# Kernel tuning notes

Measured on AMD Instinct MI355X. Metric: run time of the kernel, lower is better.

Reference implementation:

```python
import jax, jax.numpy as jnp
import numpy as np

D_MODEL = 1024
NUM_TILES = 64
TPC = 8                      # tiles_per_cluster
NUM_CLUSTERS = NUM_TILES // TPC
GRID = 16
COMP_H = 256                 # compress hidden = d_model // 4
NUM_KNOTS = 8
EPS_LN = 1e-5


def setup_inputs() -> dict:
    key = jax.random.key(0)
    ks = jax.random.split(key, 12)
    B, T = 4, 4096
    x = jax.random.normal(ks[0], (B, T, D_MODEL), dtype=jnp.float32)
    signatures_raw = jax.random.normal(ks[1], (NUM_TILES, D_MODEL), dtype=jnp.float32) * 0.5
    knot_values = jax.nn.sigmoid(jnp.linspace(-3.0, 3.0, NUM_KNOTS).astype(jnp.float32))
    temperature = jnp.ones((1,), dtype=jnp.float32)
    # compress: Linear(d,comp_h) -> GELU -> Linear(comp_h,2) -> Tanh
    compress_w1 = jax.random.normal(ks[2], (D_MODEL, COMP_H), dtype=jnp.float32) * (1.0 / np.sqrt(D_MODEL))
    compress_b1 = jnp.zeros((COMP_H,), dtype=jnp.float32)
    compress_w2 = jax.random.normal(ks[3], (COMP_H, 2), dtype=jnp.float32) * (1.0 / np.sqrt(COMP_H))
    compress_b2 = jnp.zeros((2,), dtype=jnp.float32)
    # per-tile magnitude splines: Linear(2,grid) -> ReLU -> Linear(grid,1)
    spline_w1 = jax.random.normal(ks[4], (NUM_TILES, 2, GRID), dtype=jnp.float32) * (1.0 / np.sqrt(2.0))
    spline_b1 = jnp.zeros((NUM_TILES, GRID), dtype=jnp.float32)
    spline_w2 = jax.random.normal(ks[5], (NUM_TILES, GRID, 1), dtype=jnp.float32) * (1.0 / np.sqrt(GRID))
    spline_b2 = jnp.zeros((NUM_TILES, 1), dtype=jnp.float32)
    directions = jax.random.normal(ks[6], (NUM_TILES, D_MODEL), dtype=jnp.float32) * 0.02
    norm_gamma = jnp.ones((D_MODEL,), dtype=jnp.float32)
    norm_beta = jnp.zeros((D_MODEL,), dtype=jnp.float32)
    output_scale = jnp.ones((1,), dtype=jnp.float32) * 0.1
    return dict(x=x, signatures_raw=signatures_raw, knot_values=knot_values,
                temperature=temperature, compress_w1=compress_w1, compress_b1=compress_b1,
                compress_w2=compress_w2, compress_b2=compress_b2, spline_w1=spline_w1,
                spline_b1=spline_b1, spline_w2=spline_w2, spline_b2=spline_b2,
                directions=directions, norm_gamma=norm_gamma, norm_beta=norm_beta,
                output_scale=output_scale)


def _calibrate(scores, knots, temperature):
    # ScoreCalibrationSpline: sigmoid -> linear interpolation over knots
    K = knots.shape[0]
    normalized = jax.nn.sigmoid(scores / (temperature[0] + 1e-6))
    idx_float = normalized * (K - 1)
    idx_low = jnp.clip(idx_float.astype(jnp.int32), 0, K - 2)
    idx_high = idx_low + 1
    t = idx_float - idx_low.astype(scores.dtype)
    val_low = knots[idx_low]
    val_high = knots[idx_high]
    return val_low + t * (val_high - val_low)


def _forward(x, signatures_raw, knot_values, temperature, compress_w1, compress_b1,
             compress_w2, compress_b2, spline_w1, spline_b1, spline_w2, spline_b2,
             directions, norm_gamma, norm_beta, output_scale):
    B, T, D = x.shape
    xf = x.reshape(-1, D)  # [N, D]

    # ternary quantized signatures with straight-through estimator
    q = jnp.where(signatures_raw > 0.3, 1.0,
                  jnp.where(signatures_raw < -0.3, -1.0, 0.0)).astype(signatures_raw.dtype)
    sigs = signatures_raw + jax.lax.stop_gradient(q - signatures_raw)  # [NT, D]

    # hierarchical routing: cluster signatures = sign(mean of member sigs)
    cluster_sigs = jnp.sign(sigs.reshape(NUM_CLUSTERS, TPC, D).mean(axis=1))  # [NC, D]
    cluster_scores = xf @ cluster_sigs.T                                       # [N, NC]
    cluster_gates = _calibrate(cluster_scores, knot_values, temperature)
    cluster_idx = jnp.argmax(cluster_gates, axis=-1)                           # [N]

    # within-cluster tile selection (clusters are contiguous blocks of tiles)
    tile_scores = xf @ sigs.T                                                  # [N, NT]
    tile_gates = _calibrate(tile_scores, knot_values, temperature)
    gates_by_cluster = tile_gates.reshape(-1, NUM_CLUSTERS, TPC)
    sel_gates = jnp.take_along_axis(gates_by_cluster, cluster_idx[:, None, None],
                                    axis=1)[:, 0, :]                            # [N, TPC]
    local_idx = jnp.argmax(sel_gates, axis=-1)
    tile_idx = cluster_idx * TPC + local_idx                                    # [N]

    # compress to 2D spline coordinates
    h = jax.nn.gelu(xf @ compress_w1 + compress_b1, approximate=False)
    comp = jnp.tanh(h @ compress_w2 + compress_b2)                              # [N, 2]

    # batched per-token tiny spline MLP (gather selected tile's weights)
    w1 = spline_w1[tile_idx]                                                    # [N, 2, G]
    b1 = spline_b1[tile_idx]                                                    # [N, G]
    hh = jax.nn.relu(jnp.einsum('ni,nig->ng', comp, w1) + b1)                   # [N, G]
    w2 = spline_w2[tile_idx]                                                    # [N, G, 1]
    b2 = spline_b2[tile_idx]                                                    # [N, 1]
    mag = jnp.einsum('ng,ngo->no', hh, w2) + b2                                 # [N, 1]

    ffn_out = mag * directions[tile_idx] * output_scale[0]                      # [N, D]

    # residual + LayerNorm (dropout in eval mode = identity)
    y = xf + ffn_out
    mu = y.mean(axis=-1, keepdims=True)
    var = ((y - mu) ** 2).mean(axis=-1, keepdims=True)
    y = (y - mu) / jnp.sqrt(var + EPS_LN) * norm_gamma + norm_beta
    return y.reshape(B, T, D)


def reference(x, signatures_raw, knot_values, temperature, compress_w1, compress_b1,
              compress_w2, compress_b2, spline_w1, spline_b1, spline_w2, spline_b2,
              directions, norm_gamma, norm_beta, output_scale):
    return _forward(x, signatures_raw, knot_values, temperature, compress_w1, compress_b1,
                    compress_w2, compress_b2, spline_w1, spline_b1, spline_w2, spline_b2,
                    directions, norm_gamma, norm_beta, output_scale)
```

## Files before the change

### kernel.cpp

```cpp
#include <hip/hip_runtime.h>
#include <hip/hip_bf16.h>
#include <cmath>

#define N_TOK 16384
#define DM    1024
#define CH    256
#define SGRID 16
#define NTP   24

typedef __attribute__((ext_vector_type(8))) short short8;
typedef __attribute__((ext_vector_type(4))) float floatx4;

__device__ __forceinline__ unsigned short f2bf(float f) {
  union { float f; unsigned int u; } v; v.f = f;
  unsigned int r = v.u + 0x7FFFu + ((v.u >> 16) & 1u);
  return (unsigned short)(r >> 16);
}

__device__ __forceinline__ short8 cvt8(float4 u, float4 v) {
  union { short8 s; __hip_bfloat162 h[4]; } r;
  r.h[0] = __float22bfloat162_rn(make_float2(u.x, u.y));
  r.h[1] = __float22bfloat162_rn(make_float2(u.z, u.w));
  r.h[2] = __float22bfloat162_rn(make_float2(v.x, v.y));
  r.h[3] = __float22bfloat162_rn(make_float2(v.z, v.w));
  return r.s;
}

__device__ __forceinline__ float bf2f(unsigned short b) {
  union { unsigned int u; float f; } v; v.u = ((unsigned int)b) << 16; return v.f;
}

__device__ __forceinline__ float calibrate(float s, const float* __restrict__ kn, float temp_eff) {
  float nrm = 1.0f / (1.0f + expf(-s / temp_eff));
  float idxf = nrm * 7.0f;
  int il = (int)idxf; if (il > 6) il = 6;
  float tt = idxf - (float)il;
  float lo = kn[il], hi = kn[il + 1];
  return lo + tt * (hi - lo);
}

__global__ __launch_bounds__(256) void prep_kernel(
    const float* __restrict__ sig_raw, const float* __restrict__ w1,
    unsigned short* __restrict__ wsB) {
  __shared__ float Wt[32][260];
  __shared__ float St[64][33];
  int kk = blockIdx.x, tid = threadIdx.x;
  {
    int r = tid >> 3, c0 = (tid & 7) * 32;
    const float* src = w1 + (size_t)(kk * 32 + r) * CH + c0;
#pragma unroll
    for (int i = 0; i < 8; ++i)
      *(float4*)(&Wt[r][c0 + 4 * i]) = *(const float4*)(src + 4 * i);
  }
  {
    int t = tid >> 2, c0 = (tid & 3) * 8;
    const float* src = sig_raw + (size_t)t * DM + kk * 32 + c0;
#pragma unroll
    for (int i = 0; i < 8; ++i) {
      float rr = src[i];
      St[t][c0 + i] = (rr > 0.3f) ? 1.f : ((rr < -0.3f) ? -1.f : 0.f);
    }
  }
  __syncthreads();
#pragma unroll
  for (int i = 0; i < 4; ++i) {
    int idx = i * 256 + tid;
    int nt = idx >> 6, lane = idx & 63;
    int q = lane >> 4, l = lane & 15;
    short8 v;
#pragma unroll
    for (int j = 0; j < 8; ++j) v[j] = (short)f2bf(Wt[q * 8 + j][nt * 16 + l]);
    *(short8*)(wsB + ((size_t)(kk * NTP + nt) * 64 + lane) * 8) = v;
  }
#pragma unroll
  for (int i = 0; i < 2; ++i) {
    int idx = i * 256 + tid;
    if (idx < 320) {
      int nt = 16 + (idx >> 6), lane = idx & 63;
      int q = lane >> 4, l = lane & 15;
      int n = nt * 16 + l;
      short8 v;
#pragma unroll
      for (int j = 0; j < 8; ++j) {
        int kl = q * 8 + j;
        float val = 0.f;
        if (n < 264) {
          float s = 0.f;
#pragma unroll
          for (int m = 0; m < 8; ++m) s += St[(n - 256) * 8 + m][kl];
          val = (s > 0.f) ? 1.f : ((s < 0.f) ? -1.f : 0.f);
        } else if (n < 328) {
          val = St[n - 264][kl];
        }
        v[j] = (short)f2bf(val);
      }
      *(short8*)(wsB + ((size_t)(kk * NTP + nt) * 64 + lane) * 8) = v;
    }
  }
}


#define LOADK(kk, b0, b1, av)                                               \
  {                                                                         \
    const char* bp = bBase + (size_t)(kk) * (NTP * 1024);                   \
    b0 = *(const short8*)(bp);                                              \
    if (wave < 5) b1 = *(const short8*)(bp + 16384);                        \
    unsigned cpos = ((unsigned)((kk) * 4 + quad) ^ sw) << 3;                \
    _Pragma("unroll") for (int mt = 0; mt < 4; ++mt)                        \
        av[mt] = *(const short8*)(Xsh + mt * 16384 + arow + cpos);          \
  }

#define COMPUTE(b0, b1, av)                                                 \
  {                                                                         \
    _Pragma("unroll") for (int mt = 0; mt < 4; ++mt)                        \
      acc0[mt] = __builtin_amdgcn_mfma_f32_16x16x32_bf16(av[mt], b0, acc0[mt], 0, 0, 0); \
    if (wave < 5) {                                                         \
      _Pragma("unroll") for (int mt = 0; mt < 4; ++mt)                      \
        acc1[mt] = __builtin_amdgcn_mfma_f32_16x16x32_bf16(av[mt], b1, acc1[mt], 0, 0, 0); \
    }                                                                       \
  }

__global__ __launch_bounds__(1024, 4) void fused_kernel(
    const float* __restrict__ x, const unsigned short* __restrict__ wsB,
    const float* __restrict__ b1v, const float* __restrict__ w2,
    const float* __restrict__ b2, const float* __restrict__ knots,
    const float* __restrict__ temperature, const float* __restrict__ sw1,
    const float* __restrict__ sb1, const float* __restrict__ sw2,
    const float* __restrict__ sb2, const float* __restrict__ dirs,
    const float* __restrict__ gma, const float* __restrict__ bta,
    const float* __restrict__ oscale, float* __restrict__ out) {
  __shared__ unsigned short Xsh[64 * 1024];
  __shared__ float Ssc[64][73];
  __shared__ float Psh[16][64][2];
  __shared__ float ScaleS[64];
  __shared__ int   TidxS[64];

  int tid = threadIdx.x;
  int wave = tid >> 6, lane = tid & 63, quad = lane >> 4, l15 = lane & 15;
  int m0 = blockIdx.x * 64;

  {
    const float* base = x + (size_t)m0 * DM;
#pragma unroll
    for (int i2 = 0; i2 < 8; ++i2) {
      int cg = tid + 1024 * i2;
      float4 p = *(const float4*)(base + cg * 8);
      float4 q = *(const float4*)(base + cg * 8 + 4);
      int row = cg >> 7, cir = cg & 127;
      int pos = cir ^ (row & 7);
      *(short8*)(Xsh + row * 1024 + pos * 8) = cvt8(p, q);
    }
  }
  __syncthreads();

  floatx4 acc0[4], acc1[4];
#pragma unroll
  for (int mt = 0; mt < 4; ++mt) {
    acc0[mt] = (floatx4){0.f, 0.f, 0.f, 0.f};
    acc1[mt] = (floatx4){0.f, 0.f, 0.f, 0.f};
  }

  const char* bBase = (const char*)wsB + wave * 1024 + lane * 16;
  int arow = l15 * 1024;
  unsigned sw = (unsigned)(l15 & 7);

  short8 bA0, bA1, bB0, bB1, aA[4], aB_[4];
  LOADK(0, bA0, bA1, aA);
#pragma unroll 1
  for (int kk = 0; kk < 30; kk += 2) {
    LOADK(kk + 1, bB0, bB1, aB_);
    COMPUTE(bA0, bA1, aA);
    LOADK(kk + 2, bA0, bA1, aA);
    COMPUTE(bB0, bB1, aB_);
  }
  LOADK(31, bB0, bB1, aB_);
  COMPUTE(bA0, bA1, aA);
  COMPUTE(bB0, bB1, aB_);

  if (wave < 5) {
    int sc = wave * 16 + l15;
    if (sc < 72) {
#pragma unroll
      for (int mt = 0; mt < 4; ++mt)
#pragma unroll
        for (int r = 0; r < 4; ++r)
          Ssc[mt * 16 + quad * 4 + r][sc] = acc1[mt][r];
    }
  }

  {
    int col = wave * 16 + l15;
    float b1c = b1v[col], w20 = w2[2 * col], w21 = w2[2 * col + 1];
    float q0[4][4], q1[4][4];
#pragma unroll
    for (int mt = 0; mt < 4; ++mt)
#pragma unroll
      for (int r = 0; r < 4; ++r) {
        float hh = acc0[mt][r] + b1c;
        hh = 0.5f * hh * (1.0f + erff(hh * 0.7071067811865475f));
        q0[mt][r] = hh * w20;
        q1[mt][r] = hh * w21;
      }
#pragma unroll
    for (int m = 1; m < 16; m <<= 1)
#pragma unroll
      for (int mt = 0; mt < 4; ++mt)
#pragma unroll
        for (int r = 0; r < 4; ++r) {
          q0[mt][r] += __shfl_xor(q0[mt][r], m);
          q1[mt][r] += __shfl_xor(q1[mt][r], m);
        }
    if (l15 == 0) {
#pragma unroll
      for (int mt = 0; mt < 4; ++mt)
#pragma unroll
        for (int r = 0; r < 4; ++r) {
          Psh[wave][mt * 16 + quad * 4 + r][0] = q0[mt][r];
          Psh[wave][mt * 16 + quad * 4 + r][1] = q1[mt][r];
        }
    }
  }
  __syncthreads();

  if (tid < 64) {
    int row = tid;
    float s0 = b2[0], s1 = b2[1];
#pragma unroll
    for (int j = 0; j < 16; ++j) {
      s0 += Psh[j][row][0];
      s1 += Psh[j][row][1];
    }
    float c0 = tanhf(s0), c1 = tanhf(s1);

    float temp_eff = temperature[0] + 1e-6f;
    int cid = 0; float best = -1e30f;
#pragma unroll
    for (int c = 0; c < 8; ++c) {
      float g = calibrate(Ssc[row][c], knots, temp_eff);
      if (g > best) { best = g; cid = c; }
    }
    int lidx = 0; best = -1e30f;
#pragma unroll
    for (int j = 0; j < 8; ++j) {
      float g = calibrate(Ssc[row][8 + cid * 8 + j], knots, temp_eff);
      if (g > best) { best = g; lidx = j; }
    }
    int t = cid * 8 + lidx;

    float mag = sb2[t];
#pragma unroll
    for (int g2 = 0; g2 < SGRID; ++g2) {
      float hv = c0 * sw1[t * 32 + g2] + c1 * sw1[t * 32 + 16 + g2] + sb1[t * 16 + g2];
      hv = fmaxf(hv, 0.f);
      mag += hv * sw2[t * 16 + g2];
    }
    ScaleS[row] = mag * oscale[0];
    TidxS[row] = t;
  }
  __syncthreads();

#pragma unroll 1
  for (int rr = 0; rr < 4; ++rr) {
    int row = wave * 4 + rr;
    int r7 = row & 7;
    float scale = ScaleS[row];
    const float* dr = dirs + (size_t)TidxS[row] * DM + lane * 16;
    const unsigned short* xrow = Xsh + row * 1024;
    short8 h0 = *(const short8*)(xrow + (unsigned)((2 * lane) ^ r7) * 8);
    short8 h1 = *(const short8*)(xrow + (unsigned)((2 * lane + 1) ^ r7) * 8);
    float fv[16];
    float ssum = 0.f, ssq = 0.f;
#pragma unroll
    for (int i = 0; i < 4; ++i) {
      float4 d4 = *(const float4*)(dr + 4 * i);
      float xa = bf2f((unsigned short)((i < 2 ? h0[i * 4 + 0] : h1[(i - 2) * 4 + 0])));
      float xb = bf2f((unsigned short)((i < 2 ? h0[i * 4 + 1] : h1[(i - 2) * 4 + 1])));
      float xc = bf2f((unsigned short)((i < 2 ? h0[i * 4 + 2] : h1[(i - 2) * 4 + 2])));
      float xd = bf2f((unsigned short)((i < 2 ? h0[i * 4 + 3] : h1[(i - 2) * 4 + 3])));
      fv[4 * i + 0] = xa + scale * d4.x;
      fv[4 * i + 1] = xb + scale * d4.y;
      fv[4 * i + 2] = xc + scale * d4.z;
      fv[4 * i + 3] = xd + scale * d4.w;
      ssum += fv[4 * i + 0] + fv[4 * i + 1] + fv[4 * i + 2] + fv[4 * i + 3];
      ssq += fv[4 * i + 0] * fv[4 * i + 0] + fv[4 * i + 1] * fv[4 * i + 1]
           + fv[4 * i + 2] * fv[4 * i + 2] + fv[4 * i + 3] * fv[4 * i + 3];
    }
#pragma unroll
    for (int m = 1; m < 64; m <<= 1) {
      ssum += __shfl_xor(ssum, m);
      ssq += __shfl_xor(ssq, m);
    }
    float mu = ssum * (1.0f / 1024.0f);
    float var = ssq * (1.0f / 1024.0f) - mu * mu;
    float inv = rsqrtf(var + 1e-5f);
    float* orow = out + (size_t)(m0 + row) * DM + lane * 16;
    const float* gp = gma + lane * 16;
    const float* bp2 = bta + lane * 16;
#pragma unroll
    for (int i = 0; i < 4; ++i) {
      float4 g4 = *(const float4*)(gp + 4 * i);
      float4 b4 = *(const float4*)(bp2 + 4 * i);
      float4 o;
      o.x = (fv[4 * i + 0] - mu) * inv * g4.x + b4.x;
      o.y = (fv[4 * i + 1] - mu) * inv * g4.y + b4.y;
      o.z = (fv[4 * i + 2] - mu) * inv * g4.z + b4.z;
      o.w = (fv[4 * i + 3] - mu) * inv * g4.w + b4.w;
      *(float4*)(orow + 4 * i) = o;
    }
  }
}

extern "C" void kernel_launch(void* const* d_in, const int* in_sizes, int n_in,
                              void* d_out, int out_size, void* d_ws, size_t ws_size,
                              hipStream_t stream) {
  const float* x      = (const float*)d_in[0];
  const float* sigraw = (const float*)d_in[1];
  const float* knots  = (const float*)d_in[2];
  const float* temp   = (const float*)d_in[3];
  const float* cw1    = (const float*)d_in[4];
  const float* cb1    = (const float*)d_in[5];
  const float* cw2    = (const float*)d_in[6];
  const float* cb2    = (const float*)d_in[7];
  const float* sw1    = (const float*)d_in[8];
  const float* sb1    = (const float*)d_in[9];
  const float* sw2    = (const float*)d_in[10];
  const float* sb2    = (const float*)d_in[11];
  const float* dirs   = (const float*)d_in[12];
  const float* gma    = (const float*)d_in[13];
  const float* bta    = (const float*)d_in[14];
  const float* oscale = (const float*)d_in[15];
  float* out = (float*)d_out;

  unsigned short* wsB = (unsigned short*)d_ws;

  hipLaunchKernelGGL(prep_kernel, dim3(32), dim3(256), 0, stream,
                     sigraw, cw1, wsB);
  hipLaunchKernelGGL(fused_kernel, dim3(N_TOK / 64), dim3(1024), 0, stream,
                     x, wsB, cb1, cw2, cb2, knots, temp,
                     sw1, sb1, sw2, sb2, dirs, gma, bta, oscale, out);
}
```

Baseline: 174.5 us.

## Halve token tile to 32 rows with 8 waves each covering two hidden column tiles

The fused kernel now processes 32 tokens per block with 512 threads instead of 64 tokens with 1024 threads. Each wave computes two compress-hidden column tiles plus an optional score tile over two M-tiles, and the partial GELU-projection sums are combined across both column tiles. The x staging loop first issues all global loads, then converts and stores them to LDS. Halving the LDS footprint and doubling the grid aims to raise blocks per CU and occupancy, at the cost of reloading the B operand (weights and signatures) twice as often per token.

```diff
diff --git a/kernel.cpp b/kernel.cpp
--- a/kernel.cpp
+++ b/kernel.cpp
@@ -100,27 +100,30 @@
 }
 
 
-#define LOADK(kk, b0, b1, av)                                               \
+#define LOADK(kk, b0, b1, b2r, av)                                          \
   {                                                                         \
     const char* bp = bBase + (size_t)(kk) * (NTP * 1024);                   \
     b0 = *(const short8*)(bp);                                              \
-    if (wave < 5) b1 = *(const short8*)(bp + 16384);                        \
+    b1 = *(const short8*)(bp + 8192);                                       \
+    if (wave < 5) b2r = *(const short8*)(bp + 16384);                       \
     unsigned cpos = ((unsigned)((kk) * 4 + quad) ^ sw) << 3;                \
-    _Pragma("unroll") for (int mt = 0; mt < 4; ++mt)                        \
+    _Pragma("unroll") for (int mt = 0; mt < 2; ++mt)                        \
         av[mt] = *(const short8*)(Xsh + mt * 16384 + arow + cpos);          \
   }
 
-#define COMPUTE(b0, b1, av)                                                 \
+#define COMPUTE(b0, b1, b2r, av)                                            \
   {                                                                         \
-    _Pragma("unroll") for (int mt = 0; mt < 4; ++mt)                        \
+    _Pragma("unroll") for (int mt = 0; mt < 2; ++mt) {                      \
       acc0[mt] = __builtin_amdgcn_mfma_f32_16x16x32_bf16(av[mt], b0, acc0[mt], 0, 0, 0); \
+      acc1[mt] = __builtin_amdgcn_mfma_f32_16x16x32_bf16(av[mt], b1, acc1[mt], 0, 0, 0); \
+    }                                                                       \
     if (wave < 5) {                                                         \
-      _Pragma("unroll") for (int mt = 0; mt < 4; ++mt)                      \
-        acc1[mt] = __builtin_amdgcn_mfma_f32_16x16x32_bf16(av[mt], b1, acc1[mt], 0, 0, 0); \
+      _Pragma("unroll") for (int mt = 0; mt < 2; ++mt)                      \
+        acc2[mt] = __builtin_amdgcn_mfma_f32_16x16x32_bf16(av[mt], b2r, acc2[mt], 0, 0, 0); \
     }                                                                       \
   }
 
-__global__ __launch_bounds__(1024, 4) void fused_kernel(
+__global__ __launch_bounds__(512, 4) void fused_kernel(
     const float* __restrict__ x, const unsigned short* __restrict__ wsB,
     const float* __restrict__ b1v, const float* __restrict__ w2,
     const float* __restrict__ b2, const float* __restrict__ knots,
@@ -129,82 +132,92 @@
     const float* __restrict__ sb2, const float* __restrict__ dirs,
     const float* __restrict__ gma, const float* __restrict__ bta,
     const float* __restrict__ oscale, float* __restrict__ out) {
-  __shared__ unsigned short Xsh[64 * 1024];
-  __shared__ float Ssc[64][73];
-  __shared__ float Psh[16][64][2];
-  __shared__ float ScaleS[64];
-  __shared__ int   TidxS[64];
+  __shared__ unsigned short Xsh[32 * 1024];
+  __shared__ float Ssc[32][73];
+  __shared__ float Psh[8][32][2];
+  __shared__ float ScaleS[32];
+  __shared__ int   TidxS[32];
 
   int tid = threadIdx.x;
   int wave = tid >> 6, lane = tid & 63, quad = lane >> 4, l15 = lane & 15;
-  int m0 = blockIdx.x * 64;
+  int m0 = blockIdx.x * 32;
 
   {
     const float* base = x + (size_t)m0 * DM;
+    float4 pr[8], qr[8];
 #pragma unroll
     for (int i2 = 0; i2 < 8; ++i2) {
-      int cg = tid + 1024 * i2;
-      float4 p = *(const float4*)(base + cg * 8);
-      float4 q = *(const float4*)(base + cg * 8 + 4);
+      int cg = tid + 512 * i2;
+      pr[i2] = *(const float4*)(base + cg * 8);
+      qr[i2] = *(const float4*)(base + cg * 8 + 4);
+    }
+#pragma unroll
+    for (int i2 = 0; i2 < 8; ++i2) {
+      int cg = tid + 512 * i2;
       int row = cg >> 7, cir = cg & 127;
       int pos = cir ^ (row & 7);
-      *(short8*)(Xsh + row * 1024 + pos * 8) = cvt8(p, q);
+      *(short8*)(Xsh + row * 1024 + pos * 8) = cvt8(pr[i2], qr[i2]);
     }
   }
   __syncthreads();
 
-  floatx4 acc0[4], acc1[4];
-#pragma unroll
-  for (int mt = 0; mt < 4; ++mt) {
+  floatx4 acc0[2], acc1[2], acc2[2];
+#pragma unroll
+  for (int mt = 0; mt < 2; ++mt) {
     acc0[mt] = (floatx4){0.f, 0.f, 0.f, 0.f};
     acc1[mt] = (floatx4){0.f, 0.f, 0.f, 0.f};
+    acc2[mt] = (floatx4){0.f, 0.f, 0.f, 0.f};
   }
 
   const char* bBase = (const char*)wsB + wave * 1024 + lane * 16;
   int arow = l15 * 1024;
   unsigned sw = (unsigned)(l15 & 7);
 
-  short8 bA0, bA1, bB0, bB1, aA[4], aB_[4];
-  LOADK(0, bA0, bA1, aA);
+  short8 bA0, bA1, bA2, bB0, bB1, bB2, aA[2], aB_[2];
+  LOADK(0, bA0, bA1, bA2, aA);
 #pragma unroll 1
   for (int kk = 0; kk < 30; kk += 2) {
-    LOADK(kk + 1, bB0, bB1, aB_);
-    COMPUTE(bA0, bA1, aA);
-    LOADK(kk + 2, bA0, bA1, aA);
-    COMPUTE(bB0, bB1, aB_);
-  }
-  LOADK(31, bB0, bB1, aB_);
-  COMPUTE(bA0, bA1, aA);
-  COMPUTE(bB0, bB1, aB_);
+    LOADK(kk + 1, bB0, bB1, bB2, aB_);
+    COMPUTE(bA0, bA1, bA2, aA);
+    LOADK(kk + 2, bA0, bA1, bA2, aA);
+    COMPUTE(bB0, bB1, bB2, aB_);
+  }
+  LOADK(31, bB0, bB1, bB2, aB_);
+  COMPUTE(bA0, bA1, bA2, aA);
+  COMPUTE(bB0, bB1, bB2, aB_);
 
   if (wave < 5) {
     int sc = wave * 16 + l15;
     if (sc < 72) {
 #pragma unroll
-      for (int mt = 0; mt < 4; ++mt)
+      for (int mt = 0; mt < 2; ++mt)
 #pragma unroll
         for (int r = 0; r < 4; ++r)
-          Ssc[mt * 16 + quad * 4 + r][sc] = acc1[mt][r];
+          Ssc[mt * 16 + quad * 4 + r][sc] = acc2[mt][r];
     }
   }
 
   {
-    int col = wave * 16 + l15;
-    float b1c = b1v[col], w20 = w2[2 * col], w21 = w2[2 * col + 1];
-    float q0[4][4], q1[4][4];
-#pragma unroll
-    for (int mt = 0; mt < 4; ++mt)
+    int colA = wave * 16 + l15;
+    int colB = 128 + wave * 16 + l15;
+    float b1cA = b1v[colA], w20A = w2[2 * colA], w21A = w2[2 * colA + 1];
+    float b1cB = b1v[colB], w20B = w2[2 * colB], w21B = w2[2 * colB + 1];
+    float q0[2][4], q1[2][4];
+#pragma unroll
+    for (int mt = 0; mt < 2; ++mt)
 #pragma unroll
       for (int r = 0; r < 4; ++r) {
-        float hh = acc0[mt][r] + b1c;
-        hh = 0.5f * hh * (1.0f + erff(hh * 0.7071067811865475f));
-        q0[mt][r] = hh * w20;
-        q1[mt][r] = hh * w21;
+        float hA = acc0[mt][r] + b1cA;
+        hA = 0.5f * hA * (1.0f + erff(hA * 0.7071067811865475f));
+        float hB = acc1[mt][r] + b1cB;
+        hB = 0.5f * hB * (1.0f + erff(hB * 0.7071067811865475f));
+        q0[mt][r] = hA * w20A + hB * w20B;
+        q1[mt][r] = hA * w21A + hB * w21B;
       }
 #pragma unroll
     for (int m = 1; m < 16; m <<= 1)
 #pragma unroll
-      for (int mt = 0; mt < 4; ++mt)
+      for (int mt = 0; mt < 2; ++mt)
 #pragma unroll
         for (int r = 0; r < 4; ++r) {
           q0[mt][r] += __shfl_xor(q0[mt][r], m);
@@ -212,7 +225,7 @@
         }
     if (l15 == 0) {
 #pragma unroll
-      for (int mt = 0; mt < 4; ++mt)
+      for (int mt = 0; mt < 2; ++mt)
 #pragma unroll
         for (int r = 0; r < 4; ++r) {
           Psh[wave][mt * 16 + quad * 4 + r][0] = q0[mt][r];
@@ -222,11 +235,11 @@
   }
   __syncthreads();
 
-  if (tid < 64) {
+  if (tid < 32) {
     int row = tid;
     float s0 = b2[0], s1 = b2[1];
 #pragma unroll
-    for (int j = 0; j < 16; ++j) {
+    for (int j = 0; j < 8; ++j) {
       s0 += Psh[j][row][0];
       s1 += Psh[j][row][1];
     }
@@ -335,7 +348,7 @@
 
   hipLaunchKernelGGL(prep_kernel, dim3(32), dim3(256), 0, stream,
                      sigraw, cw1, wsB);
-  hipLaunchKernelGGL(fused_kernel, dim3(N_TOK / 64), dim3(1024), 0, stream,
+  hipLaunchKernelGGL(fused_kernel, dim3(N_TOK / 32), dim3(512), 0, stream,
                      x, wsB, cb1, cw2, cb2, knots, temp,
                      sw1, sb1, sw2, sb2, dirs, gma, bta, oscale, out);
 }
```

Result: no change. 173.2 us (-0.7%).

## Split 64-token block into two 32-token halves to overlap stages

Applied to the files above, without the earlier changes.

Each workgroup now processes its 64 tokens as two 32-row halves. Both halves of x are loaded into registers up front. The second half is written to shared memory while routing for the first half runs, and the LayerNorm output of the first half can overlap the second half's MFMA loop. This aims to hide global-load and epilogue latency behind compute. In exchange it adds barriers, raises register pressure from holding 16 float4 values, and reuses the B-weight loads over 32 rows instead of 64, so weight traffic doubles.

```diff
diff --git a/kernel.cpp b/kernel.cpp
--- a/kernel.cpp
+++ b/kernel.cpp
@@ -100,23 +100,158 @@
 }
 
 
-#define LOADK(kk, b0, b1, av)                                               \
+#define LOADK(XBASE, kk, b0, b2r, av)                                       \
   {                                                                         \
     const char* bp = bBase + (size_t)(kk) * (NTP * 1024);                   \
     b0 = *(const short8*)(bp);                                              \
-    if (wave < 5) b1 = *(const short8*)(bp + 16384);                        \
+    if (wave < 5) b2r = *(const short8*)(bp + 16384);                       \
     unsigned cpos = ((unsigned)((kk) * 4 + quad) ^ sw) << 3;                \
-    _Pragma("unroll") for (int mt = 0; mt < 4; ++mt)                        \
-        av[mt] = *(const short8*)(Xsh + mt * 16384 + arow + cpos);          \
-  }
-
-#define COMPUTE(b0, b1, av)                                                 \
+    _Pragma("unroll") for (int mt = 0; mt < 2; ++mt)                        \
+        av[mt] = *(const short8*)((XBASE) + mt * 16384 + arow + cpos);      \
+  }
+
+#define COMPUTE(b0, b2r, av)                                                \
   {                                                                         \
-    _Pragma("unroll") for (int mt = 0; mt < 4; ++mt)                        \
+    _Pragma("unroll") for (int mt = 0; mt < 2; ++mt)                        \
       acc0[mt] = __builtin_amdgcn_mfma_f32_16x16x32_bf16(av[mt], b0, acc0[mt], 0, 0, 0); \
     if (wave < 5) {                                                         \
-      _Pragma("unroll") for (int mt = 0; mt < 4; ++mt)                      \
-        acc1[mt] = __builtin_amdgcn_mfma_f32_16x16x32_bf16(av[mt], b1, acc1[mt], 0, 0, 0); \
+      _Pragma("unroll") for (int mt = 0; mt < 2; ++mt)                      \
+        acc2[mt] = __builtin_amdgcn_mfma_f32_16x16x32_bf16(av[mt], b2r, acc2[mt], 0, 0, 0); \
+    }                                                                       \
+  }
+
+#define KLOOP(XBASE)                                                        \
+  {                                                                         \
+    _Pragma("unroll") for (int mt = 0; mt < 2; ++mt) {                      \
+      acc0[mt] = (floatx4){0.f, 0.f, 0.f, 0.f};                             \
+      acc2[mt] = (floatx4){0.f, 0.f, 0.f, 0.f};                             \
+    }                                                                       \
+    LOADK(XBASE, 0, bA0, bA2, aA);                                          \
+    _Pragma("unroll 1") for (int kk = 0; kk < 30; kk += 2) {                \
+      LOADK(XBASE, kk + 1, bB0, bB2, aB_);                                  \
+      COMPUTE(bA0, bA2, aA);                                                \
+      LOADK(XBASE, kk + 2, bA0, bA2, aA);                                   \
+      COMPUTE(bB0, bB2, aB_);                                               \
+    }                                                                       \
+    LOADK(XBASE, 31, bB0, bB2, aB_);                                        \
+    COMPUTE(bA0, bA2, aA);                                                  \
+    COMPUTE(bB0, bB2, aB_);                                                 \
+    if (wave < 5) {                                                         \
+      int sc = wave * 16 + l15;                                             \
+      if (sc < 72) {                                                        \
+        _Pragma("unroll") for (int mt = 0; mt < 2; ++mt)                    \
+          _Pragma("unroll") for (int r = 0; r < 4; ++r)                     \
+            Ssc[mt * 16 + quad * 4 + r][sc] = acc2[mt][r];                  \
+      }                                                                     \
+    }                                                                       \
+    {                                                                       \
+      float q0[2][4], q1[2][4];                                             \
+      _Pragma("unroll") for (int mt = 0; mt < 2; ++mt)                      \
+        _Pragma("unroll") for (int r = 0; r < 4; ++r) {                     \
+          float hh = acc0[mt][r] + b1c;                                     \
+          hh = 0.5f * hh * (1.0f + erff(hh * 0.7071067811865475f));         \
+          q0[mt][r] = hh * w20;                                             \
+          q1[mt][r] = hh * w21;                                             \
+        }                                                                   \
+      _Pragma("unroll") for (int m = 1; m < 16; m <<= 1)                    \
+        _Pragma("unroll") for (int mt = 0; mt < 2; ++mt)                    \
+          _Pragma("unroll") for (int r = 0; r < 4; ++r) {                   \
+            q0[mt][r] += __shfl_xor(q0[mt][r], m);                          \
+            q1[mt][r] += __shfl_xor(q1[mt][r], m);                          \
+          }                                                                 \
+      if (l15 == 0) {                                                       \
+        _Pragma("unroll") for (int mt = 0; mt < 2; ++mt)                    \
+          _Pragma("unroll") for (int r = 0; r < 4; ++r) {                   \
+            Psh[wave][mt * 16 + quad * 4 + r][0] = q0[mt][r];               \
+            Psh[wave][mt * 16 + quad * 4 + r][1] = q1[mt][r];               \
+          }                                                                 \
+      }                                                                     \
+    }                                                                       \
+  }
+
+#define STWRITE(XBASE, RV)                                                  \
+  _Pragma("unroll") for (int i = 0; i < 4; ++i) {                           \
+    int cg = tid + 1024 * i;                                                \
+    int row = cg >> 7, cir = cg & 127;                                      \
+    int pos = cir ^ (row & 7);                                              \
+    *(short8*)((XBASE) + row * 1024 + pos * 8) = cvt8(RV[2 * i], RV[2 * i + 1]); \
+  }
+
+#define ROUTE()                                                             \
+  if (tid < 32) {                                                           \
+    int row = tid;                                                          \
+    float s0 = b2[0], s1 = b2[1];                                           \
+    _Pragma("unroll") for (int j = 0; j < 16; ++j) {                        \
+      s0 += Psh[j][row][0];                                                 \
+      s1 += Psh[j][row][1];                                                 \
+    }                                                                       \
+    float c0 = tanhf(s0), c1 = tanhf(s1);                                   \
+    float temp_eff = temperature[0] + 1e-6f;                                \
+    int cid = 0; float best = -1e30f;                                       \
+    _Pragma("unroll") for (int c = 0; c < 8; ++c) {                         \
+      float g = calibrate(Ssc[row][c], knots, temp_eff);                    \
+      if (g > best) { best = g; cid = c; }                                  \
+    }                                                                       \
+    int lidx = 0; best = -1e30f;                                            \
+    _Pragma("unroll") for (int j = 0; j < 8; ++j) {                         \
+      float g = calibrate(Ssc[row][8 + cid * 8 + j], knots, temp_eff);      \
+      if (g > best) { best = g; lidx = j; }                                 \
+    }                                                                       \
+    int t = cid * 8 + lidx;                                                 \
+    float mag = sb2[t];                                                     \
+    _Pragma("unroll") for (int g2 = 0; g2 < SGRID; ++g2) {                  \
+      float hv = c0 * sw1[t * 32 + g2] + c1 * sw1[t * 32 + 16 + g2] + sb1[t * 16 + g2]; \
+      hv = fmaxf(hv, 0.f);                                                  \
+      mag += hv * sw2[t * 16 + g2];                                         \
+    }                                                                       \
+    ScaleS[row] = mag * oscale[0];                                          \
+    TidxS[row] = t;                                                         \
+  }
+
+#define LNOUT(XBASE, TOKBASE)                                               \
+  _Pragma("unroll 1") for (int rr = 0; rr < 2; ++rr) {                      \
+    int row = wave * 2 + rr;                                                \
+    int r7 = row & 7;                                                       \
+    float scale = ScaleS[row];                                              \
+    const float* dr = dirs + (size_t)TidxS[row] * DM + lane * 16;           \
+    const unsigned short* xrow = (XBASE) + row * 1024;                      \
+    short8 h0 = *(const short8*)(xrow + (unsigned)((2 * lane) ^ r7) * 8);   \
+    short8 h1 = *(const short8*)(xrow + (unsigned)((2 * lane + 1) ^ r7) * 8); \
+    float fv[16];                                                           \
+    float ssum = 0.f, ssq = 0.f;                                            \
+    _Pragma("unroll") for (int i = 0; i < 4; ++i) {                         \
+      float4 d4 = *(const float4*)(dr + 4 * i);                             \
+      float xa = bf2f((unsigned short)((i < 2 ? h0[i * 4 + 0] : h1[(i - 2) * 4 + 0]))); \
+      float xb = bf2f((unsigned short)((i < 2 ? h0[i * 4 + 1] : h1[(i - 2) * 4 + 1]))); \
+      float xc = bf2f((unsigned short)((i < 2 ? h0[i * 4 + 2] : h1[(i - 2) * 4 + 2]))); \
+      float xd = bf2f((unsigned short)((i < 2 ? h0[i * 4 + 3] : h1[(i - 2) * 4 + 3]))); \
+      fv[4 * i + 0] = xa + scale * d4.x;                                    \
+      fv[4 * i + 1] = xb + scale * d4.y;                                    \
+      fv[4 * i + 2] = xc + scale * d4.z;                                    \
+      fv[4 * i + 3] = xd + scale * d4.w;                                    \
+      ssum += fv[4 * i + 0] + fv[4 * i + 1] + fv[4 * i + 2] + fv[4 * i + 3]; \
+      ssq += fv[4 * i + 0] * fv[4 * i + 0] + fv[4 * i + 1] * fv[4 * i + 1]  \
+           + fv[4 * i + 2] * fv[4 * i + 2] + fv[4 * i + 3] * fv[4 * i + 3]; \
+    }                                                                       \
+    _Pragma("unroll") for (int m = 1; m < 64; m <<= 1) {                    \
+      ssum += __shfl_xor(ssum, m);                                          \
+      ssq += __shfl_xor(ssq, m);                                            \
+    }                                                                       \
+    float mu = ssum * (1.0f / 1024.0f);                                     \
+    float var = ssq * (1.0f / 1024.0f) - mu * mu;                           \
+    float inv = rsqrtf(var + 1e-5f);                                        \
+    float* orow = out + (size_t)((TOKBASE) + row) * DM + lane * 16;         \
+    const float* gp = gma + lane * 16;                                      \
+    const float* bp2 = bta + lane * 16;                                     \
+    _Pragma("unroll") for (int i = 0; i < 4; ++i) {                         \
+      float4 g4 = *(const float4*)(gp + 4 * i);                             \
+      float4 b4 = *(const float4*)(bp2 + 4 * i);                            \
+      float4 o;                                                             \
+      o.x = (fv[4 * i + 0] - mu) * inv * g4.x + b4.x;                       \
+      o.y = (fv[4 * i + 1] - mu) * inv * g4.y + b4.y;                       \
+      o.z = (fv[4 * i + 2] - mu) * inv * g4.z + b4.z;                       \
+      o.w = (fv[4 * i + 3] - mu) * inv * g4.w + b4.w;                       \
+      *(float4*)(orow + 4 * i) = o;                                         \
     }                                                                       \
   }
 
@@ -129,185 +264,60 @@
     const float* __restrict__ sb2, const float* __restrict__ dirs,
     const float* __restrict__ gma, const float* __restrict__ bta,
     const float* __restrict__ oscale, float* __restrict__ out) {
-  __shared__ unsigned short Xsh[64 * 1024];
-  __shared__ float Ssc[64][73];
-  __shared__ float Psh[16][64][2];
-  __shared__ float ScaleS[64];
-  __shared__ int   TidxS[64];
+  __shared__ unsigned short Xsh[2][32 * 1024];
+  __shared__ float Ssc[32][73];
+  __shared__ float Psh[16][32][2];
+  __shared__ float ScaleS[32];
+  __shared__ int   TidxS[32];
 
   int tid = threadIdx.x;
   int wave = tid >> 6, lane = tid & 63, quad = lane >> 4, l15 = lane & 15;
   int m0 = blockIdx.x * 64;
 
-  {
-    const float* base = x + (size_t)m0 * DM;
-#pragma unroll
-    for (int i2 = 0; i2 < 8; ++i2) {
-      int cg = tid + 1024 * i2;
-      float4 p = *(const float4*)(base + cg * 8);
-      float4 q = *(const float4*)(base + cg * 8 + 4);
-      int row = cg >> 7, cir = cg & 127;
-      int pos = cir ^ (row & 7);
-      *(short8*)(Xsh + row * 1024 + pos * 8) = cvt8(p, q);
-    }
-  }
-  __syncthreads();
-
-  floatx4 acc0[4], acc1[4];
-#pragma unroll
-  for (int mt = 0; mt < 4; ++mt) {
-    acc0[mt] = (floatx4){0.f, 0.f, 0.f, 0.f};
-    acc1[mt] = (floatx4){0.f, 0.f, 0.f, 0.f};
-  }
-
+  const float* base = x + (size_t)m0 * DM;
+  float4 ra[8], rb[8];
+#pragma unroll
+  for (int i = 0; i < 4; ++i) {
+    int cg = tid + 1024 * i;
+    ra[2 * i]     = *(const float4*)(base + cg * 8);
+    ra[2 * i + 1] = *(const float4*)(base + cg * 8 + 4);
+  }
+#pragma unroll
+  for (int i = 0; i < 4; ++i) {
+    int cg = tid + 1024 * i;
+    rb[2 * i]     = *(const float4*)(base + 32768 + cg * 8);
+    rb[2 * i + 1] = *(const float4*)(base + 32768 + cg * 8 + 4);
+  }
+  __builtin_amdgcn_sched_barrier(0);
+
+  STWRITE(&Xsh[0][0], ra);
+  __syncthreads();
+
+  int colC = wave * 16 + l15;
+  float b1c = b1v[colC], w20 = w2[2 * colC], w21 = w2[2 * colC + 1];
+
+  floatx4 acc0[2], acc2[2];
   const char* bBase = (const char*)wsB + wave * 1024 + lane * 16;
   int arow = l15 * 1024;
   unsigned sw = (unsigned)(l15 & 7);
-
-  short8 bA0, bA1, bB0, bB1, aA[4], aB_[4];
-  LOADK(0, bA0, bA1, aA);
-#pragma unroll 1
-  for (int kk = 0; kk < 30; kk += 2) {
-    LOADK(kk + 1, bB0, bB1, aB_);
-    COMPUTE(bA0, bA1, aA);
-    LOADK(kk + 2, bA0, bA1, aA);
-    COMPUTE(bB0, bB1, aB_);
-  }
-  LOADK(31, bB0, bB1, aB_);
-  COMPUTE(bA0, bA1, aA);
-  COMPUTE(bB0, bB1, aB_);
-
-  if (wave < 5) {
-    int sc = wave * 16 + l15;
-    if (sc < 72) {
-#pragma unroll
-      for (int mt = 0; mt < 4; ++mt)
-#pragma unroll
-        for (int r = 0; r < 4; ++r)
-          Ssc[mt * 16 + quad * 4 + r][sc] = acc1[mt][r];
-    }
-  }
-
-  {
-    int col = wave * 16 + l15;
-    float b1c = b1v[col], w20 = w2[2 * col], w21 = w2[2 * col + 1];
-    float q0[4][4], q1[4][4];
-#pragma unroll
-    for (int mt = 0; mt < 4; ++mt)
-#pragma unroll
-      for (int r = 0; r < 4; ++r) {
-        float hh = acc0[mt][r] + b1c;
-        hh = 0.5f * hh * (1.0f + erff(hh * 0.7071067811865475f));
-        q0[mt][r] = hh * w20;
-        q1[mt][r] = hh * w21;
-      }
-#pragma unroll
-    for (int m = 1; m < 16; m <<= 1)
-#pragma unroll
-      for (int mt = 0; mt < 4; ++mt)
-#pragma unroll
-        for (int r = 0; r < 4; ++r) {
-          q0[mt][r] += __shfl_xor(q0[mt][r], m);
-          q1[mt][r] += __shfl_xor(q1[mt][r], m);
-        }
-    if (l15 == 0) {
-#pragma unroll
-      for (int mt = 0; mt < 4; ++mt)
-#pragma unroll
-        for (int r = 0; r < 4; ++r) {
-          Psh[wave][mt * 16 + quad * 4 + r][0] = q0[mt][r];
-          Psh[wave][mt * 16 + quad * 4 + r][1] = q1[mt][r];
-        }
-    }
-  }
-  __syncthreads();
-
-  if (tid < 64) {
-    int row = tid;
-    float s0 = b2[0], s1 = b2[1];
-#pragma unroll
-    for (int j = 0; j < 16; ++j) {
-      s0 += Psh[j][row][0];
-      s1 += Psh[j][row][1];
-    }
-    float c0 = tanhf(s0), c1 = tanhf(s1);
-
-    float temp_eff = temperature[0] + 1e-6f;
-    int cid = 0; float best = -1e30f;
-#pragma unroll
-    for (int c = 0; c < 8; ++c) {
-      float g = calibrate(Ssc[row][c], knots, temp_eff);
-      if (g > best) { best = g; cid = c; }
-    }
-    int lidx = 0; best = -1e30f;
-#pragma unroll
-    for (int j = 0; j < 8; ++j) {
-      float g = calibrate(Ssc[row][8 + cid * 8 + j], knots, temp_eff);
-      if (g > best) { best = g; lidx = j; }
-    }
-    int t = cid * 8 + lidx;
-
-    float mag = sb2[t];
-#pragma unroll
-    for (int g2 = 0; g2 < SGRID; ++g2) {
-      float hv = c0 * sw1[t * 32 + g2] + c1 * sw1[t * 32 + 16 + g2] + sb1[t * 16 + g2];
-      hv = fmaxf(hv, 0.f);
-      mag += hv * sw2[t * 16 + g2];
-    }
-    ScaleS[row] = mag * oscale[0];
-    TidxS[row] = t;
-  }
-  __syncthreads();
-
-#pragma unroll 1
-  for (int rr = 0; rr < 4; ++rr) {
-    int row = wave * 4 + rr;
-    int r7 = row & 7;
-    float scale = ScaleS[row];
-    const float* dr = dirs + (size_t)TidxS[row] * DM + lane * 16;
-    const unsigned short* xrow = Xsh + row * 1024;
-    short8 h0 = *(const short8*)(xrow + (unsigned)((2 * lane) ^ r7) * 8);
-    short8 h1 = *(const short8*)(xrow + (unsigned)((2 * lane + 1) ^ r7) * 8);
-    float fv[16];
-    float ssum = 0.f, ssq = 0.f;
-#pragma unroll
-    for (int i = 0; i < 4; ++i) {
-      float4 d4 = *(const float4*)(dr + 4 * i);
-      float xa = bf2f((unsigned short)((i < 2 ? h0[i * 4 + 0] : h1[(i - 2) * 4 + 0])));
-      float xb = bf2f((unsigned short)((i < 2 ? h0[i * 4 + 1] : h1[(i - 2) * 4 + 1])));
-      float xc = bf2f((unsigned short)((i < 2 ? h0[i * 4 + 2] : h1[(i - 2) * 4 + 2])));
-      float xd = bf2f((unsigned short)((i < 2 ? h0[i * 4 + 3] : h1[(i - 2) * 4 + 3])));
-      fv[4 * i + 0] = xa + scale * d4.x;
-      fv[4 * i + 1] = xb + scale * d4.y;
-      fv[4 * i + 2] = xc + scale * d4.z;
-      fv[4 * i + 3] = xd + scale * d4.w;
-      ssum += fv[4 * i + 0] + fv[4 * i + 1] + fv[4 * i + 2] + fv[4 * i + 3];
-      ssq += fv[4 * i + 0] * fv[4 * i + 0] + fv[4 * i + 1] * fv[4 * i + 1]
-           + fv[4 * i + 2] * fv[4 * i + 2] + fv[4 * i + 3] * fv[4 * i + 3];
-    }
-#pragma unroll
-    for (int m = 1; m < 64; m <<= 1) {
-      ssum += __shfl_xor(ssum, m);
-      ssq += __shfl_xor(ssq, m);
-    }
-    float mu = ssum * (1.0f / 1024.0f);
-    float var = ssq * (1.0f / 1024.0f) - mu * mu;
-    float inv = rsqrtf(var + 1e-5f);
-    float* orow = out + (size_t)(m0 + row) * DM + lane * 16;
-    const float* gp = gma + lane * 16;
-    const float* bp2 = bta + lane * 16;
-#pragma unroll
-    for (int i = 0; i < 4; ++i) {
-      float4 g4 = *(const float4*)(gp + 4 * i);
-      float4 b4 = *(const float4*)(bp2 + 4 * i);
-      float4 o;
-      o.x = (fv[4 * i + 0] - mu) * inv * g4.x + b4.x;
-      o.y = (fv[4 * i + 1] - mu) * inv * g4.y + b4.y;
-      o.z = (fv[4 * i + 2] - mu) * inv * g4.z + b4.z;
-      o.w = (fv[4 * i + 3] - mu) * inv * g4.w + b4.w;
-      *(float4*)(orow + 4 * i) = o;
-    }
-  }
+  short8 bA0, bA2, bB0, bB2, aA[2], aB_[2];
+
+  KLOOP(&Xsh[0][0]);
+  __syncthreads();
+
+  STWRITE(&Xsh[1][0], rb);
+  ROUTE();
+  __syncthreads();
+
+  LNOUT(&Xsh[0][0], m0);
+
+  KLOOP(&Xsh[1][0]);
+  __syncthreads();
+
+  ROUTE();
+  __syncthreads();
+
+  LNOUT(&Xsh[1][0], m0 + 32);
 }
 
 extern "C" void kernel_launch(void* const* d_in, const int* in_sizes, int n_in,
```

After: 182.9 us. 1.05x slower.

## Split fused kernel into GEMM/routing kernel and separate LayerNorm kernel

Applied to the files above, without the earlier changes.

The epilogue (residual add plus LayerNorm) moves out of the big 1024-thread GEMM kernel into a new lightweight 256-thread kernel. Per-token scale and tile index pass through workspace buffers. The LN kernel rereads x in fp32 from global memory instead of the bf16 copy in LDS, which fixes the precision of the residual. The cost is an extra 64MB read of x and one more launch, in exchange for better occupancy and coalescing in the epilogue.

```diff
diff --git a/kernel.cpp b/kernel.cpp
--- a/kernel.cpp
+++ b/kernel.cpp
@@ -24,10 +24,6 @@
   r.h[2] = __float22bfloat162_rn(make_float2(v.x, v.y));
   r.h[3] = __float22bfloat162_rn(make_float2(v.z, v.w));
   return r.s;
-}
-
-__device__ __forceinline__ float bf2f(unsigned short b) {
-  union { unsigned int u; float f; } v; v.u = ((unsigned int)b) << 16; return v.f;
 }
 
 __device__ __forceinline__ float calibrate(float s, const float* __restrict__ kn, float temp_eff) {
@@ -120,20 +116,17 @@
     }                                                                       \
   }
 
-__global__ __launch_bounds__(1024, 4) void fused_kernel(
+__global__ __launch_bounds__(1024, 4) void gemm_kernel(
     const float* __restrict__ x, const unsigned short* __restrict__ wsB,
     const float* __restrict__ b1v, const float* __restrict__ w2,
     const float* __restrict__ b2, const float* __restrict__ knots,
     const float* __restrict__ temperature, const float* __restrict__ sw1,
     const float* __restrict__ sb1, const float* __restrict__ sw2,
-    const float* __restrict__ sb2, const float* __restrict__ dirs,
-    const float* __restrict__ gma, const float* __restrict__ bta,
-    const float* __restrict__ oscale, float* __restrict__ out) {
+    const float* __restrict__ sb2, const float* __restrict__ oscale,
+    float* __restrict__ gScale, int* __restrict__ gTidx) {
   __shared__ unsigned short Xsh[64 * 1024];
   __shared__ float Ssc[64][73];
   __shared__ float Psh[16][64][2];
-  __shared__ float ScaleS[64];
-  __shared__ int   TidxS[64];
 
   int tid = threadIdx.x;
   int wave = tid >> 6, lane = tid & 63, quad = lane >> 4, l15 = lane & 15;
@@ -254,33 +247,48 @@
       hv = fmaxf(hv, 0.f);
       mag += hv * sw2[t * 16 + g2];
     }
-    ScaleS[row] = mag * oscale[0];
-    TidxS[row] = t;
-  }
-  __syncthreads();
-
-#pragma unroll 1
-  for (int rr = 0; rr < 4; ++rr) {
-    int row = wave * 4 + rr;
-    int r7 = row & 7;
-    float scale = ScaleS[row];
-    const float* dr = dirs + (size_t)TidxS[row] * DM + lane * 16;
-    const unsigned short* xrow = Xsh + row * 1024;
-    short8 h0 = *(const short8*)(xrow + (unsigned)((2 * lane) ^ r7) * 8);
-    short8 h1 = *(const short8*)(xrow + (unsigned)((2 * lane + 1) ^ r7) * 8);
+    gScale[m0 + row] = mag * oscale[0];
+    gTidx[m0 + row] = t;
+  }
+}
+
+__global__ __launch_bounds__(256, 8) void ln_kernel(
+    const float* __restrict__ x, const float* __restrict__ dirs,
+    const float* __restrict__ gma, const float* __restrict__ bta,
+    const float* __restrict__ gScale, const int* __restrict__ gTidx,
+    float* __restrict__ out) {
+  int tid = threadIdx.x;
+  int wave = tid >> 6, lane = tid & 63;
+  int tok0 = blockIdx.x * 16 + wave * 4;
+
+  float4 g4[4], b4[4];
+#pragma unroll
+  for (int i = 0; i < 4; ++i) {
+    g4[i] = *(const float4*)(gma + (i * 64 + lane) * 4);
+    b4[i] = *(const float4*)(bta + (i * 64 + lane) * 4);
+  }
+
+#pragma unroll 2
+  for (int it = 0; it < 4; ++it) {
+    int tok = tok0 + it;
+    float scale = gScale[tok];
+    int t = gTidx[tok];
+    const float* xr = x + (size_t)tok * DM;
+    const float* dr = dirs + (size_t)t * DM;
+    float4 xv[4], dv[4];
+#pragma unroll
+    for (int i = 0; i < 4; ++i) {
+      xv[i] = *(const float4*)(xr + (i * 64 + lane) * 4);
+      dv[i] = *(const float4*)(dr + (i * 64 + lane) * 4);
+    }
     float fv[16];
     float ssum = 0.f, ssq = 0.f;
 #pragma unroll
     for (int i = 0; i < 4; ++i) {
-      float4 d4 = *(const float4*)(dr + 4 * i);
-      float xa = bf2f((unsigned short)((i < 2 ? h0[i * 4 + 0] : h1[(i - 2) * 4 + 0])));
-      float xb = bf2f((unsigned short)((i < 2 ? h0[i * 4 + 1] : h1[(i - 2) * 4 + 1])));
-      float xc = bf2f((unsigned short)((i < 2 ? h0[i * 4 + 2] : h1[(i - 2) * 4 + 2])));
-      float xd = bf2f((unsigned short)((i < 2 ? h0[i * 4 + 3] : h1[(i - 2) * 4 + 3])));
-      fv[4 * i + 0] = xa + scale * d4.x;
-      fv[4 * i + 1] = xb + scale * d4.y;
-      fv[4 * i + 2] = xc + scale * d4.z;
-      fv[4 * i + 3] = xd + scale * d4.w;
+      fv[4 * i + 0] = xv[i].x + scale * dv[i].x;
+      fv[4 * i + 1] = xv[i].y + scale * dv[i].y;
+      fv[4 * i + 2] = xv[i].z + scale * dv[i].z;
+      fv[4 * i + 3] = xv[i].w + scale * dv[i].w;
       ssum += fv[4 * i + 0] + fv[4 * i + 1] + fv[4 * i + 2] + fv[4 * i + 3];
       ssq += fv[4 * i + 0] * fv[4 * i + 0] + fv[4 * i + 1] * fv[4 * i + 1]
            + fv[4 * i + 2] * fv[4 * i + 2] + fv[4 * i + 3] * fv[4 * i + 3];
@@ -293,19 +301,15 @@
     float mu = ssum * (1.0f / 1024.0f);
     float var = ssq * (1.0f / 1024.0f) - mu * mu;
     float inv = rsqrtf(var + 1e-5f);
-    float* orow = out + (size_t)(m0 + row) * DM + lane * 16;
-    const float* gp = gma + lane * 16;
-    const float* bp2 = bta + lane * 16;
+    float* orow = out + (size_t)tok * DM;
 #pragma unroll
     for (int i = 0; i < 4; ++i) {
-      float4 g4 = *(const float4*)(gp + 4 * i);
-      float4 b4 = *(const float4*)(bp2 + 4 * i);
       float4 o;
-      o.x = (fv[4 * i + 0] - mu) * inv * g4.x + b4.x;
-      o.y = (fv[4 * i + 1] - mu) * inv * g4.y + b4.y;
-      o.z = (fv[4 * i + 2] - mu) * inv * g4.z + b4.z;
-      o.w = (fv[4 * i + 3] - mu) * inv * g4.w + b4.w;
-      *(float4*)(orow + 4 * i) = o;
+      o.x = (fv[4 * i + 0] - mu) * inv * g4[i].x + b4[i].x;
+      o.y = (fv[4 * i + 1] - mu) * inv * g4[i].y + b4[i].y;
+      o.z = (fv[4 * i + 2] - mu) * inv * g4[i].z + b4[i].z;
+      o.w = (fv[4 * i + 3] - mu) * inv * g4[i].w + b4[i].w;
+      *(float4*)(orow + (i * 64 + lane) * 4) = o;
     }
   }
 }
@@ -332,10 +336,14 @@
   float* out = (float*)d_out;
 
   unsigned short* wsB = (unsigned short*)d_ws;
+  float* gScale = (float*)((char*)d_ws + 1572864);
+  int*   gTidx  = (int*)((char*)d_ws + 1572864 + 65536);
 
   hipLaunchKernelGGL(prep_kernel, dim3(32), dim3(256), 0, stream,
                      sigraw, cw1, wsB);
-  hipLaunchKernelGGL(fused_kernel, dim3(N_TOK / 64), dim3(1024), 0, stream,
+  hipLaunchKernelGGL(gemm_kernel, dim3(N_TOK / 64), dim3(1024), 0, stream,
                      x, wsB, cb1, cw2, cb2, knots, temp,
-                     sw1, sb1, sw2, sb2, dirs, gma, bta, oscale, out);
-}
+                     sw1, sb1, sw2, sb2, oscale, gScale, gTidx);
+  hipLaunchKernelGGL(ln_kernel, dim3(N_TOK / 16), dim3(256), 0, stream,
+                     x, dirs, gma, bta, gScale, gTidx, out);
+}
```

After: 217.1 us. 1.24x slower.
